# Kernel tuning notes

Measured on AMD Instinct MI355X. Metric: run time of the kernel, lower is better.

The kernel has to match this reference:

```python
import jax, jax.numpy as jnp
import numpy as np

NUM_CLASSES = 8
ALPHA, GAMMA = 0.25, 2.0
EOS_COEF = 0.1
W_CE, W_BBOX, W_GIOU, W_CARD = 1.0, 5.0, 2.0, 1.0


def _build_empty_weight():
    class_counts = {0: 5158, 1: 102619, 2: 9545, 3: 9995, 4: 319, 5: 1128, 6: 729, 7: 2538}
    beta = 0.9999
    eff = {k: (1.0 - beta ** v) / (1.0 - beta) for k, v in class_counts.items()}
    total = sum(class_counts.values())
    inv = {k: total / v for k, v in class_counts.items()}
    mx = max(inv.values())
    ew = np.ones(NUM_CLASSES + 1, dtype=np.float32)
    for k in range(NUM_CLASSES):
        ew[k] = (inv[k] / mx) * (eff[4] / eff[k])
    ew[-1] = EOS_COEF
    return jnp.asarray(ew)


def setup_inputs() -> dict:
    key = jax.random.key(0)
    k1, k2, k3, k4, k5 = jax.random.split(key, 5)
    B, Q, C, Nt = 1024, 900, NUM_CLASSES, 32
    return {
        'pred_logits': jax.random.normal(k1, (B, Q, C), dtype=jnp.float32),
        'pred_boxes': jax.random.uniform(k2, (B, Q, 4), dtype=jnp.float32),
        'tgt_boxes': jax.random.uniform(k3, (B, Nt, 4), dtype=jnp.float32),
        'src_idx': jax.random.randint(k4, (B, Nt), 0, Q),
        'tgt_labels': jax.random.randint(k5, (B, Nt), 0, C),
        'empty_weight': _build_empty_weight(),
    }


def _cxcywh_to_xyxy(b):
    cx, cy, w, h = b[..., 0], b[..., 1], b[..., 2], b[..., 3]
    return jnp.stack([cx - 0.5 * w, cy - 0.5 * h, cx + 0.5 * w, cy + 0.5 * h], axis=-1)


def _paired_giou(a, b):
    # a, b: [N,4] xyxy; returns diag(generalized_box_iou(a,b)) without NxN matrix
    area_a = (a[:, 2] - a[:, 0]) * (a[:, 3] - a[:, 1])
    area_b = (b[:, 2] - b[:, 0]) * (b[:, 3] - b[:, 1])
    lt = jnp.maximum(a[:, :2], b[:, :2])
    rb = jnp.minimum(a[:, 2:], b[:, 2:])
    wh = jnp.clip(rb - lt, 0.0)
    inter = wh[:, 0] * wh[:, 1]
    union = area_a + area_b - inter
    iou = inter / union
    lt_e = jnp.minimum(a[:, :2], b[:, :2])
    rb_e = jnp.maximum(a[:, 2:], b[:, 2:])
    wh_e = jnp.clip(rb_e - lt_e, 0.0)
    area_e = wh_e[:, 0] * wh_e[:, 1]
    return iou - (area_e - union) / area_e


def reference(pred_logits, pred_boxes, tgt_boxes, src_idx, tgt_labels, empty_weight):
    B, Q, C = pred_logits.shape
    Nt = src_idx.shape[1]
    num_boxes = jnp.asarray(B * Nt, dtype=jnp.float32)
    bidx = jnp.arange(B)[:, None]

    # ---- labels: scatter matched labels, background = C ----
    target_classes = jnp.full((B, Q), C, dtype=jnp.int32).at[bidx, src_idx].set(tgt_labels.astype(jnp.int32))
    onehot = jax.nn.one_hot(target_classes, C, dtype=pred_logits.dtype)  # background -> all zeros
    # stable BCE-with-logits, elementwise focal
    bce = jnp.maximum(pred_logits, 0.0) - pred_logits * onehot + jnp.log1p(jnp.exp(-jnp.abs(pred_logits)))
    p = jax.nn.sigmoid(pred_logits)
    pt = jnp.where(onehot == 1.0, p, 1.0 - p)
    focal = jnp.where(onehot == 1.0, ALPHA, 1.0 - ALPHA) * (1.0 - pt) ** GAMMA * bce
    cls_w = empty_weight[jnp.clip(target_classes, 0, empty_weight.shape[0] - 1)]
    loss_ce = jnp.sum(focal * cls_w[..., None]) / (num_boxes + 1e-8)

    # ---- boxes: gather matched predictions ----
    src_boxes = pred_boxes[bidx, src_idx]            # [B,Nt,4]
    l1 = jnp.abs(src_boxes - tgt_boxes)
    rare = (tgt_labels == 4) | (tgt_labels == 5) | (tgt_labels == 6)
    scales = jnp.where(rare, 2.0, 1.0).astype(pred_boxes.dtype)  # [B,Nt]
    loss_bbox = jnp.sum(l1 * scales[..., None]) / (num_boxes + 1e-8)
    giou = _paired_giou(_cxcywh_to_xyxy(src_boxes.reshape(-1, 4)),
                        _cxcywh_to_xyxy(tgt_boxes.reshape(-1, 4)))
    loss_giou = jnp.sum((1.0 - giou) * scales.reshape(-1)) / (num_boxes + 1e-8)

    # ---- cardinality ----
    max_probs = jax.nn.sigmoid(pred_logits).max(axis=-1)
    card_pred = jnp.sum(max_probs > 0.5, axis=1).astype(jnp.float32)
    target_lengths = jnp.full((B,), Nt, dtype=jnp.float32)
    loss_card = jnp.mean(jnp.abs(card_pred - target_lengths))

    losses = jnp.stack([loss_ce, loss_bbox, loss_giou, loss_card])
    weights = jnp.asarray([W_CE, W_BBOX, W_GIOU, W_CARD], dtype=losses.dtype)
    return losses * weights
```

## Files before the change

kernel.cpp:

```cpp
#include <hip/hip_runtime.h>


constexpr int Bc  = 1024;
constexpr int Qc  = 900;
constexpr int Cc  = 8;
constexpr int NTc = 32;
constexpr float kAlpha = 0.25f;

__device__ inline float wave_reduce(float v) {
#pragma unroll
    for (int o = 32; o > 0; o >>= 1) v += __shfl_down(v, o, 64);
    return v;
}

__global__ __launch_bounds__(256) void detr_main(
    const float* __restrict__ logits,
    const float* __restrict__ pboxes,
    const float* __restrict__ tboxes,
    const int*   __restrict__ sidx,
    const int*   __restrict__ tlbl,
    const float* __restrict__ ew,
    float4*      __restrict__ partials)
{
    const int b   = blockIdx.x;
    const int tid = threadIdx.x;

    __shared__ int   s_src[NTc];
    __shared__ int   s_lbl[NTc];
    __shared__ float s_ew[Cc + 1];
    __shared__ float s_red[4][4];

    if (tid < NTc) {
        s_src[tid] = sidx[b * NTc + tid];
        s_lbl[tid] = tlbl[b * NTc + tid];
    }
    if (tid < Cc + 1) s_ew[tid] = ew[tid];
    __syncthreads();

    float ce = 0.f, card = 0.f;
    for (int q = tid; q < Qc; q += 256) {
        int tgt = Cc;
#pragma unroll
        for (int t = 0; t < NTc; ++t)
            if (s_src[t] == q) tgt = s_lbl[t];

        const float4* lp = (const float4*)(logits + ((size_t)(b * Qc + q)) * Cc);
        float4 xa = lp[0], xb = lp[1];
        float xs[8] = {xa.x, xa.y, xa.z, xa.w, xb.x, xb.y, xb.z, xb.w};

        float fs = 0.f, mx = -1e30f;
#pragma unroll
        for (int c = 0; c < Cc; ++c) {
            float x  = xs[c];
            mx       = fmaxf(mx, x);
            bool oh  = (c == tgt);
            float e  = __expf(-fabsf(x));
            float bce = fmaxf(x, 0.f) - (oh ? x : 0.f) + __logf(1.f + e);
            float p  = 1.f / (1.f + __expf(-x));
            float pt = oh ? p : (1.f - p);
            float om = 1.f - pt;
            fs += (oh ? kAlpha : (1.f - kAlpha)) * om * om * bce;
        }
        ce   += fs * s_ew[tgt];
        card += (mx > 0.f) ? 1.f : 0.f;
    }

    float lbb = 0.f, lgi = 0.f;
    if (tid < NTc) {
        int q = s_src[tid], lab = s_lbl[tid];
        float4 sb = *(const float4*)(pboxes + ((size_t)(b * Qc + q)) * 4);
        float4 tb = *(const float4*)(tboxes + ((size_t)(b * NTc + tid)) * 4);
        float scale = (lab == 4 || lab == 5 || lab == 6) ? 2.f : 1.f;

        lbb = (fabsf(sb.x - tb.x) + fabsf(sb.y - tb.y) +
               fabsf(sb.z - tb.z) + fabsf(sb.w - tb.w)) * scale;

        float ax0 = sb.x - 0.5f * sb.z, ay0 = sb.y - 0.5f * sb.w;
        float ax1 = sb.x + 0.5f * sb.z, ay1 = sb.y + 0.5f * sb.w;
        float bx0 = tb.x - 0.5f * tb.z, by0 = tb.y - 0.5f * tb.w;
        float bx1 = tb.x + 0.5f * tb.z, by1 = tb.y + 0.5f * tb.w;

        float areaA = (ax1 - ax0) * (ay1 - ay0);
        float areaB = (bx1 - bx0) * (by1 - by0);
        float iw = fmaxf(fminf(ax1, bx1) - fmaxf(ax0, bx0), 0.f);
        float ih = fmaxf(fminf(ay1, by1) - fmaxf(ay0, by0), 0.f);
        float inter = iw * ih;
        float uni   = areaA + areaB - inter;
        float iou   = inter / uni;
        float ewd = fmaxf(fmaxf(ax1, bx1) - fminf(ax0, bx0), 0.f);
        float ehd = fmaxf(fmaxf(ay1, by1) - fminf(ay0, by0), 0.f);
        float areaE = ewd * ehd;
        float g = iou - (areaE - uni) / areaE;
        lgi = (1.f - g) * scale;
    }

    float vals[4] = {ce, lbb, lgi, card};
    const int lane = tid & 63, wave = tid >> 6;
#pragma unroll
    for (int k = 0; k < 4; ++k) {
        float v = wave_reduce(vals[k]);
        if (lane == 0) s_red[wave][k] = v;
    }
    __syncthreads();
    if (tid == 0) {
        float4 r;
        r.x = s_red[0][0] + s_red[1][0] + s_red[2][0] + s_red[3][0];
        r.y = s_red[0][1] + s_red[1][1] + s_red[2][1] + s_red[3][1];
        r.z = s_red[0][2] + s_red[1][2] + s_red[2][2] + s_red[3][2];
        float ct = s_red[0][3] + s_red[1][3] + s_red[2][3] + s_red[3][3];
        r.w = fabsf(ct - (float)NTc);
        partials[b] = r;
    }
}

__global__ __launch_bounds__(256) void detr_finalize(
    const float4* __restrict__ partials, float* __restrict__ out)
{
    const int tid = threadIdx.x;
    __shared__ float s_red[4][4];

    float4 a = {0.f, 0.f, 0.f, 0.f};
    for (int i = tid; i < Bc; i += 256) {
        float4 p = partials[i];
        a.x += p.x; a.y += p.y; a.z += p.z; a.w += p.w;
    }
    float vals[4] = {a.x, a.y, a.z, a.w};
    const int lane = tid & 63, wave = tid >> 6;
#pragma unroll
    for (int k = 0; k < 4; ++k) {
        float v = wave_reduce(vals[k]);
        if (lane == 0) s_red[wave][k] = v;
    }
    __syncthreads();
    if (tid == 0) {
        float ce   = s_red[0][0] + s_red[1][0] + s_red[2][0] + s_red[3][0];
        float bbox = s_red[0][1] + s_red[1][1] + s_red[2][1] + s_red[3][1];
        float giou = s_red[0][2] + s_red[1][2] + s_red[2][2] + s_red[3][2];
        float card = s_red[0][3] + s_red[1][3] + s_red[2][3] + s_red[3][3];
        const float nb = (float)(Bc * NTc) + 1e-8f;
        out[0] = 1.0f * ce   / nb;
        out[1] = 5.0f * bbox / nb;
        out[2] = 2.0f * giou / nb;
        out[3] = 1.0f * card / (float)Bc;
    }
}

extern "C" void kernel_launch(void* const* d_in, const int* in_sizes, int n_in,
                              void* d_out, int out_size, void* d_ws, size_t ws_size,
                              hipStream_t stream) {
    const float* logits = (const float*)d_in[0];
    const float* pboxes = (const float*)d_in[1];
    const float* tboxes = (const float*)d_in[2];
    const int*   sidx   = (const int*)d_in[3];
    const int*   tlbl   = (const int*)d_in[4];
    const float* ew     = (const float*)d_in[5];
    float4* partials = (float4*)d_ws;

    detr_main<<<Bc, 256, 0, stream>>>(logits, pboxes, tboxes, sidx, tlbl, ew, partials);
    detr_finalize<<<1, 256, 0, stream>>>(partials, (float*)d_out);
}
```

Measured before the change: 99.74 us.

## Split each batch across two blocks, use shared query-to-label map, cheaper sigmoid

Launches two blocks per batch element, each covering half the queries, so per-thread work shrinks from up to four queries to two and more blocks are in flight. The 32-way linear scan for matched labels is replaced by a shared-memory query-to-label table filled with atomicMax, which keeps the last matching target as before. The sigmoid now reuses the exp(-|x|) term instead of a second exp. The cardinality absolute difference moves into the finalize kernel, which now sums two partials per batch; the cost is duplicated setup work in each block and twice as many partials.

```diff
diff --git a/kernel.cpp b/kernel.cpp
--- a/kernel.cpp
+++ b/kernel.cpp
@@ -5,6 +5,7 @@
 constexpr int Qc  = 900;
 constexpr int Cc  = 8;
 constexpr int NTc = 32;
+constexpr int QH  = Qc / 2;
 constexpr float kAlpha = 0.25f;
 
 __device__ inline float wave_reduce(float v) {
@@ -22,27 +23,33 @@
     const float* __restrict__ ew,
     float4*      __restrict__ partials)
 {
-    const int b   = blockIdx.x;
-    const int tid = threadIdx.x;
+    const int blk  = blockIdx.x;
+    const int b    = blk >> 1;
+    const int half = blk & 1;
+    const int tid  = threadIdx.x;
 
+    __shared__ int   s_cls[Qc];
     __shared__ int   s_src[NTc];
     __shared__ int   s_lbl[NTc];
     __shared__ float s_ew[Cc + 1];
     __shared__ float s_red[4][4];
 
+    for (int i = tid; i < Qc; i += 256) s_cls[i] = -1;
     if (tid < NTc) {
         s_src[tid] = sidx[b * NTc + tid];
         s_lbl[tid] = tlbl[b * NTc + tid];
     }
     if (tid < Cc + 1) s_ew[tid] = ew[tid];
     __syncthreads();
+    if (tid < NTc) atomicMax(&s_cls[s_src[tid]], (tid << 8) | s_lbl[tid]);
+    __syncthreads();
 
+    const int qbase = half * QH;
     float ce = 0.f, card = 0.f;
-    for (int q = tid; q < Qc; q += 256) {
-        int tgt = Cc;
-#pragma unroll
-        for (int t = 0; t < NTc; ++t)
-            if (s_src[t] == q) tgt = s_lbl[t];
+    for (int qo = tid; qo < QH; qo += 256) {
+        const int q = qbase + qo;
+        const int packed = s_cls[q];
+        const int tgt = (packed < 0) ? Cc : (packed & 0xFF);
 
         const float4* lp = (const float4*)(logits + ((size_t)(b * Qc + q)) * Cc);
         float4 xa = lp[0], xb = lp[1];
@@ -51,14 +58,16 @@
         float fs = 0.f, mx = -1e30f;
 #pragma unroll
         for (int c = 0; c < Cc; ++c) {
-            float x  = xs[c];
-            mx       = fmaxf(mx, x);
-            bool oh  = (c == tgt);
-            float e  = __expf(-fabsf(x));
-            float bce = fmaxf(x, 0.f) - (oh ? x : 0.f) + __logf(1.f + e);
-            float p  = 1.f / (1.f + __expf(-x));
-            float pt = oh ? p : (1.f - p);
-            float om = 1.f - pt;
+            float x   = xs[c];
+            mx        = fmaxf(mx, x);
+            bool  oh  = (c == tgt);
+            float e   = __expf(-fabsf(x));
+            float l1p = __logf(1.f + e);
+            float bce = fmaxf(x, 0.f) - (oh ? x : 0.f) + l1p;
+            float inv = 1.f / (1.f + e);
+            float p   = (x >= 0.f) ? inv : (1.f - inv);
+            float pt  = oh ? p : (1.f - p);
+            float om  = 1.f - pt;
             fs += (oh ? kAlpha : (1.f - kAlpha)) * om * om * bce;
         }
         ce   += fs * s_ew[tgt];
@@ -66,7 +75,7 @@
     }
 
     float lbb = 0.f, lgi = 0.f;
-    if (tid < NTc) {
+    if (half == 0 && tid < NTc) {
         int q = s_src[tid], lab = s_lbl[tid];
         float4 sb = *(const float4*)(pboxes + ((size_t)(b * Qc + q)) * 4);
         float4 tb = *(const float4*)(tboxes + ((size_t)(b * NTc + tid)) * 4);
@@ -107,9 +116,8 @@
         r.x = s_red[0][0] + s_red[1][0] + s_red[2][0] + s_red[3][0];
         r.y = s_red[0][1] + s_red[1][1] + s_red[2][1] + s_red[3][1];
         r.z = s_red[0][2] + s_red[1][2] + s_red[2][2] + s_red[3][2];
-        float ct = s_red[0][3] + s_red[1][3] + s_red[2][3] + s_red[3][3];
-        r.w = fabsf(ct - (float)NTc);
-        partials[b] = r;
+        r.w = s_red[0][3] + s_red[1][3] + s_red[2][3] + s_red[3][3];
+        partials[blk] = r;
     }
 }
 
@@ -121,8 +129,12 @@
 
     float4 a = {0.f, 0.f, 0.f, 0.f};
     for (int i = tid; i < Bc; i += 256) {
-        float4 p = partials[i];
-        a.x += p.x; a.y += p.y; a.z += p.z; a.w += p.w;
+        float4 p0 = partials[2 * i];
+        float4 p1 = partials[2 * i + 1];
+        a.x += p0.x + p1.x;
+        a.y += p0.y + p1.y;
+        a.z += p0.z + p1.z;
+        a.w += fabsf((p0.w + p1.w) - (float)NTc);
     }
     float vals[4] = {a.x, a.y, a.z, a.w};
     const int lane = tid & 63, wave = tid >> 6;
@@ -156,6 +168,6 @@
     const float* ew     = (const float*)d_in[5];
     float4* partials = (float4*)d_ws;
 
-    detr_main<<<Bc, 256, 0, stream>>>(logits, pboxes, tboxes, sidx, tlbl, ew, partials);
+    detr_main<<<2 * Bc, 256, 0, stream>>>(logits, pboxes, tboxes, sidx, tlbl, ew, partials);
     detr_finalize<<<1, 256, 0, stream>>>(partials, (float*)d_out);
 }
```

After: 97.14 us. 1.03x faster.
